# Kernel tuning notes

Hardware: AMD Instinct MI355X
Metric: run time of the kernel (lower is better)

## Reference

```python
import jax, jax.numpy as jnp
import numpy as np

NEG_SLOPE = 0.2  # PyG GATConv default LeakyReLU slope
EPS = 1e-16      # PyG softmax denominator epsilon


def _gat_layer(x, src, dst, W, a_src, a_dst, b, H, C):
    """One PyG-style GATConv layer (eval mode, add_self_loops already applied).
    x: [N, F_in], W: [F_in, H*C], a_src/a_dst: [H, C], b: [H*C]."""
    N = x.shape[0]
    h = (x @ W).reshape(N, H, C)                       # [N,H,C]
    alpha_src = jnp.sum(h * a_src, axis=-1)            # [N,H]
    alpha_dst = jnp.sum(h * a_dst, axis=-1)            # [N,H]
    e = jax.nn.leaky_relu(alpha_src[src] + alpha_dst[dst], NEG_SLOPE)  # [E,H]
    m = jax.ops.segment_max(e, dst, num_segments=N)    # [N,H] segment-softmax max
    p = jnp.exp(e - m[dst])                            # [E,H]
    s = jax.ops.segment_sum(p, dst, num_segments=N)    # [N,H]
    attn = p / (s[dst] + EPS)                          # [E,H]
    out = jax.ops.segment_sum(attn[:, :, None] * h[src], dst, num_segments=N)  # [N,H,C]
    return out.reshape(N, H * C) + b


def _add_self_loops(edge_index, N):
    loop = jnp.arange(N, dtype=edge_index.dtype)
    src = jnp.concatenate([edge_index[0], loop])
    dst = jnp.concatenate([edge_index[1], loop])
    return src, dst


def setup_inputs() -> dict:
    key = jax.random.key(0)
    N, E = 50000, 500000
    F_in, H, C = 336, 4, 128
    HC = H * C  # 512
    n_cls = 10
    ks = jax.random.split(key, 16)

    def glorot(k, shape):
        fan = shape[0] + shape[-1]
        return jax.random.normal(k, shape, jnp.float32) * jnp.sqrt(2.0 / fan)

    x = jax.random.normal(ks[0], (N, F_in), jnp.float32)
    edge_index = jax.random.randint(ks[1], (2, E), 0, N, dtype=jnp.int64)
    return {
        "x": x,
        "edge_index": edge_index,
        "W1": glorot(ks[2], (F_in, HC)),
        "a_src1": glorot(ks[3], (H, C)),
        "a_dst1": glorot(ks[4], (H, C)),
        "b1": jnp.zeros((HC,), jnp.float32),
        "W2": glorot(ks[5], (HC, HC)),
        "a_src2": glorot(ks[6], (H, C)),
        "a_dst2": glorot(ks[7], (H, C)),
        "b2": jnp.zeros((HC,), jnp.float32),
        "Wc1": glorot(ks[8], (HC, C)),
        "bc1": jnp.zeros((C,), jnp.float32),
        "Wc2": glorot(ks[9], (C, n_cls)),
        "bc2": jnp.zeros((n_cls,), jnp.float32),
    }


def reference(x, edge_index, W1, a_src1, a_dst1, b1, W2, a_src2, a_dst2, b2, Wc1, bc1, Wc2, bc2):
    H, C = 4, 128
    N = x.shape[0]
    src, dst = _add_self_loops(edge_index, N)
    h = _gat_layer(x, src, dst, W1, a_src1, a_dst1, b1, H, C)
    h = jax.nn.elu(h)  # ELU between layers only
    h = _gat_layer(h, src, dst, W2, a_src2, a_dst2, b2, H, C)
    # classifier (dropout is identity in eval)
    z = jax.nn.relu(h @ Wc1 + bc1)
    logits = z @ Wc2 + bc2
    return logits
```

## Files before the change

kernel.cpp:

```cpp
#include <hip/hip_runtime.h>
#include <math.h>

typedef unsigned short u16;
typedef unsigned int u32;
typedef short short8 __attribute__((ext_vector_type(8)));
typedef __bf16 bf16x8 __attribute__((ext_vector_type(8)));
typedef float f32x4 __attribute__((ext_vector_type(4)));
typedef u32 u32x4 __attribute__((ext_vector_type(4)));

__device__ __forceinline__ float b2f(u16 u) {
    union { u32 i; float f; } v; v.i = ((u32)u) << 16; return v.f;
}
__device__ __forceinline__ float b2f_lo(u32 q) {
    union { u32 i; float f; } v; v.i = q << 16; return v.f;
}
__device__ __forceinline__ float b2f_hi(u32 q) {
    union { u32 i; float f; } v; v.i = q & 0xffff0000u; return v.f;
}
__device__ __forceinline__ u16 f2b(float f) {
    union { float f; u32 i; } v; v.f = f;
    u32 i = v.i;
    u32 r = (i + 0x7fffu + ((i >> 16) & 1u)) >> 16;
    return (u16)r;
}
__device__ __forceinline__ u32 pack2(u16 a, u16 b) { return (u32)a | ((u32)b << 16); }


__device__ void agg_dev(const int* __restrict__ rowptr, const int* __restrict__ col,
                        const float* __restrict__ asrc, const float* __restrict__ adst,
                        const u16* __restrict__ hb, const float* __restrict__ bias,
                        u16* __restrict__ outb, int elu, int NODES) {
    const int wid = __builtin_amdgcn_readfirstlane((blockIdx.x * 256 + threadIdx.x) >> 6);
    const int nwaves = gridDim.x << 2;
    const int l = threadIdx.x & 63;
    const int hd = l >> 4;
    const int cbase = 8 * l;
    float bv[8];
#pragma unroll
    for (int c = 0; c < 8; c++) bv[c] = bias[cbase + c];

    for (int n = wid; n < NODES; n += nwaves) {
        const int beg = __builtin_amdgcn_readfirstlane(rowptr[n]);
        const int end = __builtin_amdgcn_readfirstlane(rowptr[n + 1]);
        const float ad = adst[n * 4 + hd];
        float acc0[8], acc1[8];
#pragma unroll
        for (int c = 0; c < 8; c++) { acc0[c] = 0.f; acc1[c] = 0.f; }
        float ss0 = 0.f, ss1 = 0.f;
        for (int j = beg; j < end; j += 8) {
            int s[8];
#pragma unroll
            for (int q = 0; q < 8; q++) {
                int jq = j + q;
                jq = jq < end ? jq : end - 1;
                s[q] = __builtin_amdgcn_readfirstlane(col[jq]);
            }
            u32x4 g[8];
#pragma unroll
            for (int q = 0; q < 8; q++)
                g[q] = *(const u32x4*)(hb + (size_t)s[q] * 512 + cbase);
            float p[8];
#pragma unroll
            for (int q = 0; q < 8; q++) {
                float e = asrc[(size_t)s[q] * 4 + hd] + ad;
                e = e > 0.f ? e : 0.2f * e;
                float pe = __expf(e);
                p[q] = (j + q < end) ? pe : 0.f;
            }
#pragma unroll
            for (int q = 0; q < 8; q += 2) {
                ss0 += p[q]; ss1 += p[q + 1];
#pragma unroll
                for (int u = 0; u < 4; u++) {
                    acc0[2 * u]     += p[q]     * b2f_lo(g[q][u]);
                    acc0[2 * u + 1] += p[q]     * b2f_hi(g[q][u]);
                    acc1[2 * u]     += p[q + 1] * b2f_lo(g[q + 1][u]);
                    acc1[2 * u + 1] += p[q + 1] * b2f_hi(g[q + 1][u]);
                }
            }
        }
        float inv = 1.f / (ss0 + ss1 + 1e-16f);
        float v[8];
#pragma unroll
        for (int c = 0; c < 8; c++) {
            float tv = (acc0[c] + acc1[c]) * inv + bv[c];
            if (elu) tv = tv > 0.f ? tv : expm1f(tv);
            v[c] = tv;
        }
        u32x4 ov;
        ov[0] = pack2(f2b(v[0]), f2b(v[1]));
        ov[1] = pack2(f2b(v[2]), f2b(v[3]));
        ov[2] = pack2(f2b(v[4]), f2b(v[5]));
        ov[3] = pack2(f2b(v[6]), f2b(v[7]));
        *(u32x4*)(outb + (size_t)n * 512 + cbase) = ov;
    }
}

__device__ void gemm_dev(const u16* __restrict__ A, const u16* __restrict__ Bt,
                         u16* __restrict__ C, const float* __restrict__ bias,
                         const float* __restrict__ aS, const float* __restrict__ aD,
                         float* __restrict__ asr, float* __restrict__ ads,
                         const float* __restrict__ Wc2, const float* __restrict__ bc2,
                         float* __restrict__ outp,
                         int M, int N, int K, int act, char* shm,
                         u16* As, u16* Bs, float (*red)[128][2]) {
    const int t = threadIdx.x;
    const int l = t & 63, w = t >> 6;
    const int m0 = blockIdx.x * 128, n0 = blockIdx.y * 128;
    const int sr = t >> 2;
    const int sc = (t & 3) * 8;
    const int wm = (w >> 1) * 64, wn = (w & 1) * 64;

    const int rA0 = min(m0 + sr, M - 1);
    const int rA1 = min(m0 + sr + 64, M - 1);
    const int rB0 = min(n0 + sr, N - 1);
    const int rB1 = min(n0 + sr + 64, N - 1);

    f32x4 acc[4][4];
    f32x4 z4 = {0.f, 0.f, 0.f, 0.f};
#pragma unroll
    for (int i = 0; i < 4; i++)
#pragma unroll
        for (int j = 0; j < 4; j++) acc[i][j] = z4;

    for (int k0 = 0; k0 < K; k0 += 32) {
        short8 a0 = *(const short8*)(A + (size_t)rA0 * K + k0 + sc);
        short8 a1 = *(const short8*)(A + (size_t)rA1 * K + k0 + sc);
        short8 b0 = *(const short8*)(Bt + (size_t)rB0 * K + k0 + sc);
        short8 b1 = *(const short8*)(Bt + (size_t)rB1 * K + k0 + sc);
        __syncthreads();
        *(short8*)(As + sr * 32 + sc) = a0;
        *(short8*)(As + (sr + 64) * 32 + sc) = a1;
        *(short8*)(Bs + sr * 32 + sc) = b0;
        *(short8*)(Bs + (sr + 64) * 32 + sc) = b1;
        __syncthreads();

        bf16x8 af[4], bfr[4];
#pragma unroll
        for (int i = 0; i < 4; i++) {
            af[i]  = *(const bf16x8*)(As + (wm + i * 16 + (l & 15)) * 32 + (l >> 4) * 8);
            bfr[i] = *(const bf16x8*)(Bs + (wn + i * 16 + (l & 15)) * 32 + (l >> 4) * 8);
        }
#pragma unroll
        for (int i = 0; i < 4; i++)
#pragma unroll
            for (int j = 0; j < 4; j++)
                acc[i][j] = __builtin_amdgcn_mfma_f32_16x16x32_bf16(af[i], bfr[j], acc[i][j], 0, 0, 0);
    }

    if (act == 2) {
        __syncthreads();
        float* wl = (float*)shm;
        float (*logbuf)[128][10] = (float (*)[128][10])(shm + 8192);
        for (int i = t; i < 1280; i += 256) wl[i] = Wc2[i];
        if (t < 10) wl[1280 + t] = bc2[t];
        __syncthreads();
        int cj[4];
#pragma unroll
        for (int j = 0; j < 4; j++) cj[j] = wn + j * 16 + (l & 15);
#pragma unroll
        for (int i = 0; i < 4; i++) {
#pragma unroll
            for (int r = 0; r < 4; r++) {
                float zv[4];
#pragma unroll
                for (int j = 0; j < 4; j++) {
                    float v = acc[i][j][r] + (bias ? bias[cj[j]] : 0.f);
                    zv[j] = v > 0.f ? v : 0.f;
                }
                float part[10];
#pragma unroll
                for (int k = 0; k < 10; k++) {
                    float s = 0.f;
#pragma unroll
                    for (int j = 0; j < 4; j++) s += zv[j] * wl[cj[j] * 10 + k];
#pragma unroll
                    for (int o = 1; o < 16; o <<= 1) s += __shfl_xor(s, o);
                    part[k] = s;
                }
                if ((l & 15) == 0) {
                    int rl = wm + i * 16 + (l >> 4) * 4 + r;
#pragma unroll
                    for (int k = 0; k < 10; k++) logbuf[w & 1][rl][k] = part[k];
                }
            }
        }
        __syncthreads();
        if (t < 128) {
            int row = m0 + t;
            if (row < M) {
#pragma unroll
                for (int k = 0; k < 10; k++)
                    outp[(size_t)row * 10 + k] =
                        logbuf[0][t][k] + logbuf[1][t][k] + wl[1280 + k];
            }
        }
        return;
    }

#pragma unroll
    for (int i = 0; i < 4; i++) {
        int rbase = m0 + wm + i * 16 + (l >> 4) * 4;
#pragma unroll
        for (int j = 0; j < 4; j++) {
            int c = n0 + wn + j * 16 + (l & 15);
            float bv = bias ? bias[c] : 0.f;
#pragma unroll
            for (int r = 0; r < 4; r++) {
                int row = rbase + r;
                if (row < M) {
                    float v = acc[i][j][r] + bv;
                    if (act == 1) v = v > 0.f ? v : 0.f;
                    C[(size_t)row * N + c] = f2b(v);
                }
            }
        }
    }

    if (aS) {
        const int hd = n0 >> 7;
        float aSv[4], aDv[4];
#pragma unroll
        for (int j = 0; j < 4; j++) {
            int c = n0 + wn + j * 16 + (l & 15);
            aSv[j] = aS[c];
            aDv[j] = aD[c];
        }
#pragma unroll
        for (int i = 0; i < 4; i++) {
#pragma unroll
            for (int r = 0; r < 4; r++) {
                float vs = 0.f, vd = 0.f;
#pragma unroll
                for (int j = 0; j < 4; j++) {
                    float hv = acc[i][j][r];
                    vs += hv * aSv[j];
                    vd += hv * aDv[j];
                }
#pragma unroll
                for (int o = 1; o < 16; o <<= 1) {
                    vs += __shfl_xor(vs, o);
                    vd += __shfl_xor(vd, o);
                }
                if ((l & 15) == 0) {
                    int rl = wm + i * 16 + (l >> 4) * 4 + r;
                    red[w & 1][rl][0] = vs;
                    red[w & 1][rl][1] = vd;
                }
            }
        }
        __syncthreads();
        if (t < 128) {
            int row = m0 + t;
            if (row < M) {
                asr[row * 4 + hd] = red[0][t][0] + red[1][t][0];
                ads[row * 4 + hd] = red[0][t][1] + red[1][t][1];
            }
        }
    }
}

__global__ __launch_bounds__(256) void BaselineGAT_41764261987077_kernel(
    int phase, int aux,
    const float* x, const int* ei,
    const float* W1, const float* as1, const float* ad1, const float* b1,
    const float* W2, const float* as2, const float* ad2, const float* b2,
    const float* Wc1, const float* bc1, const float* Wc2, const float* bc2,
    float* out,
    u16* hAb, u16* hbB, float* asr, float* ads,
    u16* xb, u16* w1t, u16* w2t, u16* wc1t,
    int* flag, int* cnt, int* tmp, int* bsum, int* boff,
    int* rowptr, int* cursor, int* col,
    const u16* gA, const u16* gB, u16* gC, const float* gBias,
    const float* gAs, const float* gAd,
    int gM, int gN, int gK, int gAct,
    int NODES, int E, int nblk)
{
    __shared__ f32x4 shm4[1156];
    char* shm = (char*)shm4;
    u16* As = (u16*)shm;
    u16* Bs = (u16*)(shm + 8192);
    float (*red)[128][2] = (float (*)[128][2])(shm + 16384);
    int* smi = (int*)shm;
    int* smb = (int*)(shm + 2048);

    const int t = threadIdx.x;
    const int gid = blockIdx.x * 256 + t;
    const int EN = E + NODES;

    switch (phase) {
    case 100: {
        if (gid < NODES * 10) out[gid] = 1000.0f;
    } break;
    case 0: {
        if (blockIdx.x == 0) {
            if (t == 0) smi[256] = 0;
            __syncthreads();
            for (int j = t; j < 1024; j += 256)
                if (ei[2 * j + 1] != 0) atomicAdd(&smi[256], 1);
            __syncthreads();
            if (t == 0) flag[0] = (smi[256] < 16) ? 2 : 1;
        } else {
            int i = (blockIdx.x - 1) * 256 + t;
            if (i < NODES) cnt[i] = 0;
        }
    } break;
    case 2: {
        if (gid >= EN) return;
        int step = flag[0];
        int d;
        if (gid < E) {
            d = ei[(size_t)(E + gid) * step];
            if ((unsigned)d >= (unsigned)NODES) d = 0;
        } else d = gid - E;
        atomicAdd(&cnt[d], 1);
    } break;
    case 3: {
        smi[t] = (gid < NODES) ? cnt[gid] : 0;
        __syncthreads();
        for (int o = 1; o < 256; o <<= 1) {
            int add = (t >= o) ? smi[t - o] : 0;
            __syncthreads();
            smi[t] += add;
            __syncthreads();
        }
        if (gid < NODES) tmp[gid] = smi[t];
        if (t == 255) bsum[blockIdx.x] = smi[255];
    } break;
    case 5: {
        smb[t] = (t < nblk) ? bsum[t] : 0;
        __syncthreads();
        for (int o = 1; o < 256; o <<= 1) {
            int add = (t >= o) ? smb[t - o] : 0;
            __syncthreads();
            smb[t] += add;
            __syncthreads();
        }
        int base = (blockIdx.x == 0) ? 0 : smb[blockIdx.x - 1];
        if (gid >= NODES) return;
        int incl = tmp[gid] + base;
        rowptr[gid + 1] = incl;
        cursor[gid] = incl - cnt[gid];
        if (gid == 0) rowptr[0] = 0;
    } break;
    case 6: {
        if (gid >= EN) return;
        int step = flag[0];
        int d, s;
        if (gid < E) {
            s = ei[(size_t)gid * step];
            d = ei[(size_t)(E + gid) * step];
            if ((unsigned)s >= (unsigned)NODES) s = 0;
            if ((unsigned)d >= (unsigned)NODES) d = 0;
        } else { d = gid - E; s = d; }
        int pos = atomicAdd(&cursor[d], 1);
        col[pos] = s;
    } break;
    case 20: {
        int i = gid;
        const int XC = NODES * 44;
        if (i < XC) {
            int n = i / 44, kk = (i - n * 44) * 8;
            short8 o;
            if (kk < 336) {
                const f32x4* xp = (const f32x4*)(x + (size_t)n * 336 + kk);
                f32x4 f0 = xp[0], f1 = xp[1];
                o[0] = (short)f2b(f0[0]); o[1] = (short)f2b(f0[1]);
                o[2] = (short)f2b(f0[2]); o[3] = (short)f2b(f0[3]);
                o[4] = (short)f2b(f1[0]); o[5] = (short)f2b(f1[1]);
                o[6] = (short)f2b(f1[2]); o[7] = (short)f2b(f1[3]);
            } else {
#pragma unroll
                for (int e = 0; e < 8; e++) o[e] = 0;
            }
            *(short8*)(xb + (size_t)n * 352 + kk) = o;
            return;
        }
        i -= XC;
        if (i < 512 * 352) {
            int n = i / 352, k = i - n * 352;
            w1t[i] = (k < 336) ? f2b(W1[(size_t)k * 512 + n]) : (u16)0;
            return;
        }
        i -= 512 * 352;
        if (i < 512 * 512) {
            int n = i >> 9, k = i & 511;
            w2t[i] = f2b(W2[(size_t)k * 512 + n]);
            return;
        }
        i -= 512 * 512;
        if (i < 128 * 512) {
            int n = i >> 9, k = i & 511;
            wc1t[i] = f2b(Wc1[(size_t)k * 128 + n]);
        }
    } break;
    case 30: gemm_dev(gA, gB, gC, gBias, gAs, gAd, asr, ads,
                      Wc2, bc2, out, gM, gN, gK, gAct, shm, As, Bs, red); break;
    case 31: agg_dev(rowptr, col, asr, ads, hAb, gBias, hbB, aux, NODES); break;
    }
}

extern "C" void kernel_launch(void* const* d_in, const int* in_sizes, int n_in,
                              void* d_out, int out_size, void* d_ws, size_t ws_size,
                              hipStream_t stream) {
    const float* x   = (const float*)d_in[0];
    const int*   ei  = (const int*)d_in[1];
    const float* W1  = (const float*)d_in[2];
    const float* as1 = (const float*)d_in[3];
    const float* ad1 = (const float*)d_in[4];
    const float* b1  = (const float*)d_in[5];
    const float* W2  = (const float*)d_in[6];
    const float* as2 = (const float*)d_in[7];
    const float* ad2 = (const float*)d_in[8];
    const float* b2  = (const float*)d_in[9];
    const float* Wc1 = (const float*)d_in[10];
    const float* bc1 = (const float*)d_in[11];
    const float* Wc2 = (const float*)d_in[12];
    const float* bc2 = (const float*)d_in[13];

    const int NODES = in_sizes[0] / 336;
    const int E     = in_sizes[1] / 2;

    char* ws = (char*)d_ws;
    size_t off = 0;
    auto alloc = [&](size_t b) -> char* {
        char* p = ws + off; off = (off + b + 255) & ~(size_t)255; return p;
    };
    u16*   xb   = (u16*)alloc((size_t)NODES * 352 * 2);
    u16*   hAb  = (u16*)alloc((size_t)NODES * 512 * 2);
    u16*   hbB  = (u16*)alloc((size_t)NODES * 512 * 2);
    float* asr  = (float*)alloc((size_t)NODES * 4 * 4);
    float* ads  = (float*)alloc((size_t)NODES * 4 * 4);
    u16*   w1t  = (u16*)alloc((size_t)512 * 352 * 2);
    u16*   w2t  = (u16*)alloc((size_t)512 * 512 * 2);
    u16*   wc1t = (u16*)alloc((size_t)128 * 512 * 2);
    int* flag   = (int*)alloc(256);
    int* cnt    = (int*)alloc((size_t)NODES * 4);
    int* tmp    = (int*)alloc((size_t)NODES * 4);
    int* bsum   = (int*)alloc(4096);
    int* boff   = (int*)alloc(4096);
    int* rowptr = (int*)alloc((size_t)(NODES + 1) * 4);
    int* cursor = (int*)alloc((size_t)NODES * 4);
    int* col    = (int*)alloc((size_t)(E + NODES) * 4);

    const int nblk = (NODES + 255) / 256;
    const int eblk = (E + NODES + 255) / 256;
    const int oblk = (out_size + 255) / 256;
    const int mt   = (NODES + 127) / 128;
    const int cvt_total = NODES * 44 + 512 * 352 + 512 * 512 + 128 * 512;

    auto L = [&](int phase, int aux, dim3 grid,
                 const u16* gA = nullptr, const u16* gB = nullptr,
                 u16* gC = nullptr, const float* gBias = nullptr,
                 const float* gAs = nullptr, const float* gAd = nullptr,
                 int gM = 0, int gN = 0, int gK = 0, int gAct = 0) {
        BaselineGAT_41764261987077_kernel<<<grid, 256, 0, stream>>>(
            phase, aux, x, ei, W1, as1, ad1, b1, W2, as2, ad2, b2,
            Wc1, bc1, Wc2, bc2, (float*)d_out,
            hAb, hbB, asr, ads, xb, w1t, w2t, wc1t,
            flag, cnt, tmp, bsum, boff, rowptr, cursor, col,
            gA, gB, gC, gBias, gAs, gAd, gM, gN, gK, gAct,
            NODES, E, nblk);
    };

    if (n_in < 14 || off > ws_size) { L(100, 1, oblk); return; }

    L(0, 0, nblk + 1);
    L(2, 0, eblk);
    L(3, 0, nblk);
    L(5, 0, nblk);
    L(6, 0, eblk);

    L(20, 0, (cvt_total + 255) / 256);

    L(30, 0, dim3(mt, 4), xb, w1t, hAb, nullptr, as1, ad1, NODES, 512, 352, 0);
    L(31, 1, 4096, nullptr, nullptr, nullptr, b1);

    L(30, 0, dim3(mt, 4), hbB, w2t, hAb, nullptr, as2, ad2, NODES, 512, 512, 0);
    L(31, 0, 4096, nullptr, nullptr, nullptr, b2);

    L(30, 0, dim3(mt, 1), hbB, wc1t, nullptr, bc1, nullptr, nullptr, NODES, 128, 512, 2);
}
```

Before: 598.0 us.

## Stage GEMM tiles via direct global-to-LDS loads with swizzle and XCD tile remap

The bf16 GEMM tile loads now use global_load_lds (16 bytes per lane), so data goes straight from global memory into shared memory instead of passing through registers. The LDS layout is XOR-swizzled on 8-element chunks, with matching read offsets, to cut bank conflicts on the MFMA fragment reads. Workgroup IDs are also remapped so consecutive logical tiles land on the same XCD, which should improve L2 reuse of the A/B panels. The loop is still single-buffered with two barriers per k-step, and correctness depends on the barrier waiting for the asynchronous LDS loads.

```diff
diff --git a/kernel.cpp b/kernel.cpp
--- a/kernel.cpp
+++ b/kernel.cpp
@@ -7,6 +7,13 @@
 typedef __bf16 bf16x8 __attribute__((ext_vector_type(8)));
 typedef float f32x4 __attribute__((ext_vector_type(4)));
 typedef u32 u32x4 __attribute__((ext_vector_type(4)));
+
+typedef const __attribute__((address_space(1))) void* as1cv;
+typedef __attribute__((address_space(3))) void* as3v;
+
+__device__ __forceinline__ void gload16(const void* g, void* l) {
+    __builtin_amdgcn_global_load_lds((as1cv)g, (as3v)l, 16, 0, 0);
+}
 
 __device__ __forceinline__ float b2f(u16 u) {
     union { u32 i; float f; } v; v.i = ((u32)u) << 16; return v.f;
@@ -106,15 +113,36 @@
                          u16* As, u16* Bs, float (*red)[128][2]) {
     const int t = threadIdx.x;
     const int l = t & 63, w = t >> 6;
-    const int m0 = blockIdx.x * 128, n0 = blockIdx.y * 128;
-    const int sr = t >> 2;
-    const int sc = (t & 3) * 8;
+
+    const int nwg = gridDim.x * gridDim.y;
+    const int fid = blockIdx.x + gridDim.x * blockIdx.y;
+    int logical;
+    {
+        const int q = nwg >> 3, r = nwg & 7;
+        const int xcd = fid & 7, ix = fid >> 3;
+        logical = (xcd < r ? xcd * (q + 1) : r * (q + 1) + (xcd - r) * q) + ix;
+    }
+    const int gy = gridDim.y;
+    const int mtile = logical / gy;
+    const int hd_ = logical - mtile * gy;
+    const int m0 = mtile * 128, n0 = hd_ * 128;
+
     const int wm = (w >> 1) * 64, wn = (w & 1) * 64;
 
-    const int rA0 = min(m0 + sr, M - 1);
-    const int rA1 = min(m0 + sr + 64, M - 1);
-    const int rB0 = min(n0 + sr, N - 1);
-    const int rB1 = min(n0 + sr + 64, N - 1);
+    const int rl0 = w * 32 + (l >> 2);
+    const int rl1 = rl0 + 16;
+    const int gso = 8 * ((l & 3) ^ ((l >> 3) & 3));
+    const u16* pA0 = A + (size_t)min(m0 + rl0, M - 1) * K + gso;
+    const u16* pA1 = A + (size_t)min(m0 + rl1, M - 1) * K + gso;
+    const u16* pB0 = Bt + (size_t)min(n0 + rl0, N - 1) * K + gso;
+    const u16* pB1 = Bt + (size_t)min(n0 + rl1, N - 1) * K + gso;
+    u16* lA0 = As + (size_t)(w * 32) * 32;
+    u16* lA1 = lA0 + 16 * 32;
+    u16* lB0 = Bs + (size_t)(w * 32) * 32;
+    u16* lB1 = lB0 + 16 * 32;
+
+    const int rs = ((l & 15) >> 1) & 3;
+    const int roff = 8 * ((l >> 4) ^ rs);
 
     f32x4 acc[4][4];
     f32x4 z4 = {0.f, 0.f, 0.f, 0.f};
@@ -124,22 +152,18 @@
         for (int j = 0; j < 4; j++) acc[i][j] = z4;
 
     for (int k0 = 0; k0 < K; k0 += 32) {
-        short8 a0 = *(const short8*)(A + (size_t)rA0 * K + k0 + sc);
-        short8 a1 = *(const short8*)(A + (size_t)rA1 * K + k0 + sc);
-        short8 b0 = *(const short8*)(Bt + (size_t)rB0 * K + k0 + sc);
-        short8 b1 = *(const short8*)(Bt + (size_t)rB1 * K + k0 + sc);
-        __syncthreads();
-        *(short8*)(As + sr * 32 + sc) = a0;
-        *(short8*)(As + (sr + 64) * 32 + sc) = a1;
-        *(short8*)(Bs + sr * 32 + sc) = b0;
-        *(short8*)(Bs + (sr + 64) * 32 + sc) = b1;
+        __syncthreads();
+        gload16(pA0 + k0, lA0);
+        gload16(pA1 + k0, lA1);
+        gload16(pB0 + k0, lB0);
+        gload16(pB1 + k0, lB1);
         __syncthreads();
 
         bf16x8 af[4], bfr[4];
 #pragma unroll
         for (int i = 0; i < 4; i++) {
-            af[i]  = *(const bf16x8*)(As + (wm + i * 16 + (l & 15)) * 32 + (l >> 4) * 8);
-            bfr[i] = *(const bf16x8*)(Bs + (wn + i * 16 + (l & 15)) * 32 + (l >> 4) * 8);
+            af[i]  = *(const bf16x8*)(As + (wm + i * 16 + (l & 15)) * 32 + roff);
+            bfr[i] = *(const bf16x8*)(Bs + (wn + i * 16 + (l & 15)) * 32 + roff);
         }
 #pragma unroll
         for (int i = 0; i < 4; i++)
```

Result: no change. 593.0 us (-0.8%).
